# Kernel tuning notes

Measured on AMD Instinct MI355X. Metric: run time of the kernel, lower is better.

The kernel has to match this reference:

```python
import jax, jax.numpy as jnp
import numpy as np
from jax import lax


def _conv(x, w, b, pad, dil):
    # standard dense conv, NCHW / OIHW
    out = lax.conv_general_dilated(
        x, w, window_strides=(1, 1), padding=[(pad, pad), (pad, pad)],
        rhs_dilation=(dil, dil), dimension_numbers=('NCHW', 'OIHW', 'NCHW'))
    return out + b[None, :, None, None]


def _bilinear_sample(x, py, px):
    # x: [B,C,H,W]; py,px: [B,H,W] float coords. Zero padding outside bounds
    # (matches torchvision deform_conv2d bilinear sampling).
    B, C, H, W = x.shape
    y0 = jnp.floor(py)
    x0 = jnp.floor(px)
    wy = (py - y0)[:, None]  # [B,1,H,W]
    wx = (px - x0)[:, None]
    y0i = y0.astype(jnp.int32)
    x0i = x0.astype(jnp.int32)
    xf = x.reshape(B, C, H * W)

    def gather(yi, xi):
        valid = ((yi >= 0) & (yi < H) & (xi >= 0) & (xi < W))[:, None]
        yc = jnp.clip(yi, 0, H - 1)
        xc = jnp.clip(xi, 0, W - 1)
        idx = jnp.broadcast_to((yc * W + xc).reshape(B, 1, H * W), (B, C, H * W))
        v = jnp.take_along_axis(xf, idx, axis=2).reshape(B, C, H, W)
        return v * valid.astype(x.dtype)

    v00 = gather(y0i, x0i)
    v01 = gather(y0i, x0i + 1)
    v10 = gather(y0i + 1, x0i)
    v11 = gather(y0i + 1, x0i + 1)
    return (v00 * (1 - wy) * (1 - wx) + v01 * (1 - wy) * wx
            + v10 * wy * (1 - wx) + v11 * wy * wx)


def _deform_dw_conv(x, off_w, off_b, dw_w, k, pad, dil):
    # offset net: regular conv -> [B, 2*k*k, H, W] (dy,dx per kernel tap)
    # then depthwise deformable conv with weight dw_w: [C,1,k,k], no bias.
    B, C, H, W = x.shape
    off = _conv(x, off_w, off_b, pad, dil).reshape(B, k * k, 2, H, W)
    ys = jnp.arange(H, dtype=x.dtype)[None, :, None]  # [1,H,1]
    xs = jnp.arange(W, dtype=x.dtype)[None, None, :]  # [1,1,W]
    out = jnp.zeros_like(x)
    for t in range(k * k):  # small fixed tap count (25 or 49)
        ki, kj = t // k, t % k
        py = ys - pad + ki * dil + off[:, t, 0]  # [B,H,W]
        px = xs - pad + kj * dil + off[:, t, 1]
        samp = _bilinear_sample(x, py, px)       # [B,C,H,W]
        out = out + samp * dw_w[:, 0, ki, kj][None, :, None, None]
    return out


def setup_inputs() -> dict:
    key = jax.random.key(0)
    ks = jax.random.split(key, 10)
    B, C, H, W = 8, 64, 128, 128
    x = jax.random.normal(ks[0], (B, C, H, W), dtype=jnp.float32)
    # conv0: DeformConv 5x5, pad=2, dil=1, depthwise
    off0_w = jax.random.normal(ks[1], (2 * 25, C, 5, 5), dtype=jnp.float32) * 0.01
    off0_b = jnp.zeros((2 * 25,), dtype=jnp.float32)
    dw0_w = jax.random.normal(ks[2], (C, 1, 5, 5), dtype=jnp.float32) * (1.0 / 5.0)
    # conv_spatial: DeformConv 7x7, pad=9, dil=3, depthwise
    off1_w = jax.random.normal(ks[3], (2 * 49, C, 7, 7), dtype=jnp.float32) * 0.01
    off1_b = jnp.zeros((2 * 49,), dtype=jnp.float32)
    dw1_w = jax.random.normal(ks[4], (C, 1, 7, 7), dtype=jnp.float32) * (1.0 / 7.0)
    # conv1: 1x1 dense conv with bias
    conv1_w = jax.random.normal(ks[5], (C, C, 1, 1), dtype=jnp.float32) * (1.0 / np.sqrt(C))
    conv1_b = jnp.zeros((C,), dtype=jnp.float32)
    return {"x": x, "off0_w": off0_w, "off0_b": off0_b, "dw0_w": dw0_w,
            "off1_w": off1_w, "off1_b": off1_b, "dw1_w": dw1_w,
            "conv1_w": conv1_w, "conv1_b": conv1_b}


def reference(x, off0_w, off0_b, dw0_w, off1_w, off1_b, dw1_w, conv1_w, conv1_b):
    u = x
    attn = _deform_dw_conv(x, off0_w, off0_b, dw0_w, k=5, pad=2, dil=1)
    attn = _deform_dw_conv(attn, off1_w, off1_b, dw1_w, k=7, pad=9, dil=3)
    attn = jnp.einsum('bchw,oc->bohw', attn, conv1_w[:, :, 0, 0]) + conv1_b[None, :, None, None]
    return u * attn
```

## Files before the change

### kernel.cpp

```cpp
#include <hip/hip_runtime.h>
#include <hip/hip_fp16.h>

#define Bb 8
#define C  64
#define Hh 128
#define Ww 128
#define HW (Hh * Ww)

typedef __attribute__((ext_vector_type(8))) short b16x8;
typedef __attribute__((ext_vector_type(4))) float f32x4;
typedef _Float16 f16x8 __attribute__((ext_vector_type(8)));
typedef __fp16 fp16x2cv __attribute__((ext_vector_type(2)));

__device__ __forceinline__ ushort f2h(float f) {
    union { _Float16 h; ushort u; } z; z.h = (_Float16)f; return z.u;
}
__device__ __forceinline__ uint pkrtz_u(float a, float b) {
    union { fp16x2cv h; uint u; } z;
    z.h = __builtin_amdgcn_cvt_pkrtz(a, b); return z.u;
}
__device__ __forceinline__ f16x8 s2h8(b16x8 s) {
    union { b16x8 s; f16x8 h; } x; x.s = s; return x.h;
}
__device__ __forceinline__ __half2 u2hh(uint u) {
    union { uint u; __half2 h; } x; x.u = u; return x.h;
}
__device__ __forceinline__ uint hh2u(__half2 h) {
    union { uint u; __half2 h; } x; x.h = h; return x.u;
}
__device__ __forceinline__ float h2f_lo(uint u) {
    union { uint u; __half2 h; } x; x.u = u; return __low2float(x.h);
}
__device__ __forceinline__ float h2f_hi(uint u) {
    union { uint u; __half2 h; } x; x.u = u; return __high2float(x.h);
}

__global__ void pack_nhwc(const float* __restrict__ in, ushort* __restrict__ out) {
    __shared__ ushort t[64][65];
    const int bx = blockIdx.x;
    const int b = bx >> 8, rem = bx & 255, h = rem >> 1, w0 = (rem & 1) << 6;
    const int x = threadIdx.x, wl = x & 63, cs = x >> 6;
    const float* ip = in + (((size_t)b * 64) << 14) + (h << 7) + w0 + wl;
    #pragma unroll
    for (int i = 0; i < 16; ++i) {
        const int c = i * 4 + cs;
        t[wl][c] = f2h(ip[(size_t)c << 14]);
    }
    __syncthreads();
    ushort* op = out + ((size_t)((b * Hh + h) * Ww + w0)) * 64 + wl;
    #pragma unroll
    for (int i = 0; i < 16; ++i) {
        const int w = i * 4 + cs;
        op[(size_t)w * 64] = t[w][wl];
    }
}

__global__ void pack_w(const float* __restrict__ src, ushort* __restrict__ dst,
                       int OC, int OCP, int KK, int n) {
    const int idx = blockIdx.x * 256 + threadIdx.x;
    if (idx >= n) return;
    const int kk = idx & 31;
    const int oc = (idx >> 5) % OCP;
    const int s = idx / (32 * OCP);
    const int c = (s & 1) * 32 + kk;
    const int t = s >> 1;
    const float v = (oc < OC) ? src[((size_t)oc * 64 + c) * KK + t] : 0.f;
    dst[idx] = f2h(v);
}

__global__ void pack_dwt(const float* __restrict__ src, ushort* __restrict__ dst, int KK) {
    const int i = blockIdx.x * 256 + threadIdx.x;
    if (i < KK * 64) {
        const int t = i >> 6, ch = i & 63;
        dst[i] = f2h(src[ch * KK + t]);
    }
}

template<int K, int PAD, int DIL, int OCP, int KR>
__global__ __launch_bounds__(256, 4) void conv_mfma(
    const ushort* __restrict__ xp,
    const ushort* __restrict__ wp,
    const float* __restrict__ bias,
    ushort* __restrict__ outp) {
    constexpr int WIDTH = 128 + (K - 1) * DIL;
    constexpr int S = 2 * K * K;
    constexpr int SP = S + 2;
    constexpr int NT = OCP / 16;
    constexpr int TPW = (NT + 3) / 4;
    constexpr int STG = KR * WIDTH * 64;
    constexpr int EPI = 128 * SP;
    constexpr int LN = STG > EPI ? STG : EPI;
    __shared__ __align__(16) ushort lds[LN];

    const int bx = blockIdx.x;
    const int b = bx >> 7, h = bx & 127;
    const int tid = threadIdx.x, lane = tid & 63, wid = tid >> 6;
    const int l15 = lane & 15, lg = lane >> 4;

    f32x4 acc[TPW][8] = {};

    const int nph = (K + KR - 1) / KR;
    for (int ph = 0; ph < nph; ++ph) {
        const int kr0 = ph * KR;
        const int krn = (K - kr0 < KR) ? (K - kr0) : KR;
        __syncthreads();
        const int chunks = krn * WIDTH * 8;
        for (int q = tid; q < chunks; q += 256) {
            const int ki = q / (WIDTH * 8);
            const int r2 = q - ki * (WIDTH * 8);
            const int widx = r2 >> 3, csl = r2 & 7;
            const int y = h - PAD + (kr0 + ki) * DIL;
            const int w = -PAD + widx;
            uint4 v = make_uint4(0, 0, 0, 0);
            if ((unsigned)y < 128u && (unsigned)w < 128u)
                v = *(const uint4*)(xp + (((size_t)(b * 128 + y) * 128 + w) << 6) + (csl << 3));
            ((uint4*)lds)[(ki * WIDTH + widx) * 8 + (csl ^ (widx & 7))] = v;
        }
        __syncthreads();

        const int t1 = (kr0 + krn) * K;
        for (int t = kr0 * K; t < t1; ++t) {
            const int ki = t / K - kr0;
            const int kj = t - (t / K) * K;
            const int s0 = 2 * t;
            b16x8 a[2][TPW];
            #pragma unroll
            for (int i = 0; i < TPW; ++i) {
                if (wid + 4 * i < NT) {
                    const int ot = wid + 4 * i;
                    const size_t ab = ((size_t)(ot * 16 + l15)) * 32 + lg * 8;
                    a[0][i] = *(const b16x8*)(wp + (size_t)s0 * (OCP * 32) + ab);
                    a[1][i] = *(const b16x8*)(wp + (size_t)(s0 + 1) * (OCP * 32) + ab);
                }
            }
            const int wb0 = l15 + kj * DIL;
            int idx = (ki * WIDTH + wb0) * 8 + (lg ^ (wb0 & 7));
            #pragma unroll
            for (int pt = 0; pt < 8; ++pt) {
                const b16x8 b0 = ((const b16x8*)lds)[idx];
                const b16x8 b1 = ((const b16x8*)lds)[idx ^ 4];
                #pragma unroll
                for (int i = 0; i < TPW; ++i) {
                    if (wid + 4 * i < NT) {
                        acc[i][pt] = __builtin_amdgcn_mfma_f32_16x16x32_f16(s2h8(a[0][i]), s2h8(b0), acc[i][pt], 0, 0, 0);
                        acc[i][pt] = __builtin_amdgcn_mfma_f32_16x16x32_f16(s2h8(a[1][i]), s2h8(b1), acc[i][pt], 0, 0, 0);
                    }
                }
                idx += 128;
            }
        }
    }

    __syncthreads();
    #pragma unroll
    for (int i = 0; i < TPW; ++i) {
        const int ot = wid + 4 * i;
        if (ot >= NT) continue;
        #pragma unroll
        for (int r = 0; r < 4; ++r) {
            const int oc = ot * 16 + lg * 4 + r;
            if (oc < S) {
                const float bv = bias[oc];
                #pragma unroll
                for (int pt = 0; pt < 8; ++pt)
                    lds[(pt * 16 + l15) * SP + oc] = f2h(acc[i][pt][r] + bv);
            }
        }
    }
    __syncthreads();
    constexpr int SH = S / 2, SPH = SP / 2;
    const uint* lu = (const uint*)lds;
    uint* og = (uint*)outp + ((size_t)bx << 7) * SH;
    for (int q = tid; q < 128 * SH; q += 256) {
        const int pix = q / SH, s = q - pix * SH;
        og[q] = lu[pix * SPH + s];
    }
}

template <int K, int PAD, int DIL>
__global__ __launch_bounds__(512) void deform6(
    const ushort* __restrict__ xp,
    const ushort* __restrict__ off,
    const ushort* __restrict__ dwt,
    ushort* __restrict__ outb) {
    constexpr int KK = K * K;
    constexpr int H0 = (KK + 1) / 2;
    constexpr int SSTB = 32 * KK * 16;
    __shared__ __align__(16) char smem[SSTB + KK * 128];
    uint4* sST = (uint4*)smem;
    ushort* dwl = (ushort*)(smem + SSTB);

    const int tid = threadIdx.x;
    const int pix0 = blockIdx.x * 32;

    for (int i = tid; i < KK * 32; i += 512)
        ((uint*)dwl)[i] = ((const uint*)dwt)[i];

    const uint* og = (const uint*)off + (size_t)pix0 * KK;
    for (int q = tid; q < 32 * KK; q += 512) {
        const int pl2 = q / KK, t2 = q - pl2 * KK;
        const int pix = pix0 + pl2;
        const int h = (pix >> 7) & 127, w = pix & 127;
        const uint od = og[q];
        const int ki = t2 / K, kj = t2 - ki * K;
        const float py = (float)(h - PAD + ki * DIL) + h2f_lo(od);
        const float px = (float)(w - PAD + kj * DIL) + h2f_hi(od);
        const float y0f = floorf(py), x0f = floorf(px);
        const float wy = py - y0f, wx = px - x0f;
        const int y0 = (int)y0f, x0 = (int)x0f;
        const int y1 = y0 + 1, x1 = x0 + 1;
        const float m00 = ((unsigned)y0 < 128u && (unsigned)x0 < 128u) ? 1.f : 0.f;
        const float m01 = ((unsigned)y0 < 128u && (unsigned)x1 < 128u) ? 1.f : 0.f;
        const float m10 = ((unsigned)y1 < 128u && (unsigned)x0 < 128u) ? 1.f : 0.f;
        const float m11 = ((unsigned)y1 < 128u && (unsigned)x1 < 128u) ? 1.f : 0.f;
        const int y0c = min(max(y0, 0), 127), y1c = min(max(y1, 0), 127);
        const int x0c = min(max(x0, 0), 127), x1c = min(max(x1, 0), 127);
        const float w00 = (1.f - wy) * (1.f - wx) * m00;
        const float w01 = (1.f - wy) * wx * m01;
        const float w10 = wy * (1.f - wx) * m10;
        const float w11 = wy * wx * m11;
        const uint o00b = (uint)(((y0c << 7) | x0c) << 7);
        const uint o11b = (uint)(((y1c << 7) | x1c) << 7);
        const uint dxf = (uint)(x1c - x0c) << 24;
        sST[q] = make_uint4(o00b | dxf, o11b,
                            pkrtz_u(w00, w01), pkrtz_u(w10, w11));
    }
    __syncthreads();

    const int g = tid & 7, pl = (tid >> 3) & 31, half = tid >> 8;
    const int pix = pix0 + pl;
    const int bimg = pix0 >> 14;
    const int gb2 = g << 4;
    const char* xb8 = (const char*)xp + ((size_t)bimg << 21);
    const int base = pl * KK;
    const int t0 = half ? H0 : 0, t1 = half ? KK : H0;

    __half2 acc_h[4] = {};

    for (int tt = t0; tt < t1; ++tt) {
        const uint4 st = sST[base + tt];
        const uint a = st.x;
        const uint o00 = (a & 0x00FFFFFFu) + gb2;
        const uint dxb = (a >> 17) & 128u;
        const uint o11 = st.y + gb2;
        const __half2 wv0 = u2hh(st.z), wv1 = u2hh(st.w);
        const __half2 w00b = __low2half2(wv0), w01b = __high2half2(wv0);
        const __half2 w10b = __low2half2(wv1), w11b = __high2half2(wv1);
        const uint4 qa = *(const uint4*)(xb8 + o00);
        const uint4 qb = *(const uint4*)(xb8 + (o00 + dxb));
        const uint4 qc = *(const uint4*)(xb8 + (o11 - dxb));
        const uint4 qd = *(const uint4*)(xb8 + o11);
        const uint4 dwv = *(const uint4*)(dwl + (tt << 6) + (g << 3));
        const uint* Ap = (const uint*)&qa;
        const uint* Bp = (const uint*)&qb;
        const uint* Cp = (const uint*)&qc;
        const uint* Dp = (const uint*)&qd;
        const uint* Wp = (const uint*)&dwv;
        #pragma unroll
        for (int j = 0; j < 4; ++j) {
            __half2 v = __hmul2(u2hh(Ap[j]), w00b);
            v = __hfma2(u2hh(Bp[j]), w01b, v);
            v = __hfma2(u2hh(Cp[j]), w10b, v);
            v = __hfma2(u2hh(Dp[j]), w11b, v);
            acc_h[j] = __hfma2(v, u2hh(Wp[j]), acc_h[j]);
        }
    }

    __syncthreads();
    uint4* red = (uint4*)smem;
    if (half) {
        red[tid & 255] = make_uint4(hh2u(acc_h[0]), hh2u(acc_h[1]),
                                    hh2u(acc_h[2]), hh2u(acc_h[3]));
    }
    __syncthreads();
    if (!half) {
        const uint4 o = red[tid];
        acc_h[0] = __hadd2(acc_h[0], u2hh(o.x));
        acc_h[1] = __hadd2(acc_h[1], u2hh(o.y));
        acc_h[2] = __hadd2(acc_h[2], u2hh(o.z));
        acc_h[3] = __hadd2(acc_h[3], u2hh(o.w));
        uint o4[4];
        #pragma unroll
        for (int j = 0; j < 4; ++j) o4[j] = hh2u(acc_h[j]);
        *(uint4*)(outb + ((size_t)pix << 6) + (g << 3)) = *(uint4*)o4;
    }
}

__global__ __launch_bounds__(256) void pw_mfma(
    const ushort* __restrict__ attn, const ushort* __restrict__ wp2,
    const float* __restrict__ b1, const float* __restrict__ x,
    float* __restrict__ out) {
    __shared__ __align__(16) ushort lds[64 * 64];
    const int tid = threadIdx.x, lane = tid & 63, wid = tid >> 6;
    const int l15 = lane & 15, lg = lane >> 4;
    const int pix0 = blockIdx.x << 6;

    const uint4* src = (const uint4*)(attn + ((size_t)pix0 << 6));
    for (int q = tid; q < 512; q += 256) {
        const int widx = q >> 3, csl = q & 7;
        ((uint4*)lds)[widx * 8 + (csl ^ (widx & 7))] = src[q];
    }
    __syncthreads();

    const b16x8 a0 = *(const b16x8*)(wp2 + ((size_t)(wid * 16 + l15)) * 32 + lg * 8);
    const b16x8 a1 = *(const b16x8*)(wp2 + ((size_t)(64 + wid * 16 + l15)) * 32 + lg * 8);
    f32x4 acc[4] = {};
    #pragma unroll
    for (int pt = 0; pt < 4; ++pt) {
        const int wb = pt * 16 + l15;
        const int idx = wb * 8 + (lg ^ (wb & 7));
        const b16x8 b0 = ((const b16x8*)lds)[idx];
        const b16x8 b1v = ((const b16x8*)lds)[idx ^ 4];
        acc[pt] = __builtin_amdgcn_mfma_f32_16x16x32_f16(s2h8(a0), s2h8(b0), acc[pt], 0, 0, 0);
        acc[pt] = __builtin_amdgcn_mfma_f32_16x16x32_f16(s2h8(a1), s2h8(b1v), acc[pt], 0, 0, 0);
    }

    const int b = pix0 >> 14, hw0 = pix0 & 16383;
    #pragma unroll
    for (int r = 0; r < 4; ++r) {
        const int oc = wid * 16 + lg * 4 + r;
        const float bv = b1[oc];
        const size_t base = (((size_t)b * 64 + oc) << 14) + hw0;
        #pragma unroll
        for (int pt = 0; pt < 4; ++pt) {
            const size_t oi = base + pt * 16 + l15;
            out[oi] = x[oi] * (acc[pt][r] + bv);
        }
    }
}

extern "C" void kernel_launch(void* const* d_in, const int* in_sizes, int n_in,
                              void* d_out, int out_size, void* d_ws, size_t ws_size,
                              hipStream_t stream) {
    const float* x       = (const float*)d_in[0];
    const float* off0_w  = (const float*)d_in[1];
    const float* off0_b  = (const float*)d_in[2];
    const float* dw0_w   = (const float*)d_in[3];
    const float* off1_w  = (const float*)d_in[4];
    const float* off1_b  = (const float*)d_in[5];
    const float* dw1_w   = (const float*)d_in[6];
    const float* conv1_w = (const float*)d_in[7];
    const float* conv1_b = (const float*)d_in[8];
    float* out = (float*)d_out;

    const size_t NPX = (size_t)Bb * HW;
    ushort* xp     = (ushort*)d_ws;
    ushort* attn0b = xp + NPX * 64;
    ushort* attn1b = attn0b + NPX * 64;
    ushort* offb   = attn1b + NPX * 64;
    ushort* wp0    = offb + NPX * 98;
    ushort* wp1    = wp0 + 50 * 64 * 32;
    ushort* wpP    = wp1 + 98 * 112 * 32;
    ushort* dwt0   = wpP + 2 * 64 * 32;
    ushort* dwt1   = dwt0 + 25 * 64;

    const dim3 blk(256);

    pack_nhwc<<<2048, blk, 0, stream>>>(x, xp);
    pack_w<<<(50 * 64 * 32 + 255) / 256, blk, 0, stream>>>(off0_w, wp0, 50, 64, 25, 50 * 64 * 32);
    pack_w<<<(98 * 112 * 32 + 255) / 256, blk, 0, stream>>>(off1_w, wp1, 98, 112, 49, 98 * 112 * 32);
    pack_w<<<16, blk, 0, stream>>>(conv1_w, wpP, 64, 64, 1, 2 * 64 * 32);
    pack_dwt<<<(25 * 64 + 255) / 256, blk, 0, stream>>>(dw0_w, dwt0, 25);
    pack_dwt<<<(49 * 64 + 255) / 256, blk, 0, stream>>>(dw1_w, dwt1, 49);

    conv_mfma<5, 2, 1, 64, 2><<<1024, blk, 0, stream>>>(xp, wp0, off0_b, offb);
    deform6<5, 2, 1><<<4096, 512, 0, stream>>>(xp, offb, dwt0, attn0b);

    conv_mfma<7, 9, 3, 112, 2><<<1024, blk, 0, stream>>>(attn0b, wp1, off1_b, offb);
    deform6<7, 9, 3><<<4096, 512, 0, stream>>>(attn0b, offb, dwt1, attn1b);

    pw_mfma<<<2048, blk, 0, stream>>>(attn1b, wpP, conv1_b, x, out);
}
```

Baseline: 311.6 us.

## Restructure deformable sampling to 64 pixels per block without tap split; merge pack kernels

Measured after the change: 302.2 us. -3.0%, faster.

```diff
diff --git a/kernel.cpp b/kernel.cpp
--- a/kernel.cpp
+++ b/kernel.cpp
@@ -55,10 +55,8 @@
     }
 }
 
-__global__ void pack_w(const float* __restrict__ src, ushort* __restrict__ dst,
-                       int OC, int OCP, int KK, int n) {
-    const int idx = blockIdx.x * 256 + threadIdx.x;
-    if (idx >= n) return;
+__device__ __forceinline__ void do_pack_w(const float* src, ushort* dst,
+                                          int OC, int OCP, int KK, int idx) {
     const int kk = idx & 31;
     const int oc = (idx >> 5) % OCP;
     const int s = idx / (32 * OCP);
@@ -67,13 +65,30 @@
     const float v = (oc < OC) ? src[((size_t)oc * 64 + c) * KK + t] : 0.f;
     dst[idx] = f2h(v);
 }
-
-__global__ void pack_dwt(const float* __restrict__ src, ushort* __restrict__ dst, int KK) {
-    const int i = blockIdx.x * 256 + threadIdx.x;
-    if (i < KK * 64) {
-        const int t = i >> 6, ch = i & 63;
-        dst[i] = f2h(src[ch * KK + t]);
-    }
+__global__ void pack_all(const float* __restrict__ off0_w, ushort* __restrict__ wp0,
+                         const float* __restrict__ off1_w, ushort* __restrict__ wp1,
+                         const float* __restrict__ conv1_w, ushort* __restrict__ wpP,
+                         const float* __restrict__ dw0_w, ushort* __restrict__ dwt0,
+                         const float* __restrict__ dw1_w, ushort* __restrict__ dwt1) {
+    const int N0 = 50 * 2 * 64 * 32;
+    const int n0 = 2 * 25 * 64 * 32;
+    const int n1 = 2 * 49 * 112 * 32;
+    const int n2 = 2 * 64 * 32;
+    const int n3 = 25 * 64;
+    const int n4 = 49 * 64;
+    (void)N0;
+    int idx = blockIdx.x * 256 + threadIdx.x;
+    if (idx < n0) { do_pack_w(off0_w, wp0, 50, 64, 25, idx); return; }
+    idx -= n0;
+    if (idx < n1) { do_pack_w(off1_w, wp1, 98, 112, 49, idx); return; }
+    idx -= n1;
+    if (idx < n2) { do_pack_w(conv1_w, wpP, 64, 64, 1, idx); return; }
+    idx -= n2;
+    if (idx < n3) { const int t = idx >> 6, ch = idx & 63;
+                    dwt0[idx] = f2h(dw0_w[ch * 25 + t]); return; }
+    idx -= n3;
+    if (idx < n4) { const int t = idx >> 6, ch = idx & 63;
+                    dwt1[idx] = f2h(dw1_w[ch * 49 + t]); }
 }
 
 template<int K, int PAD, int DIL, int OCP, int KR>
@@ -178,26 +193,24 @@
 }
 
 template <int K, int PAD, int DIL>
-__global__ __launch_bounds__(512) void deform6(
+__global__ __launch_bounds__(512) void deform7k(
     const ushort* __restrict__ xp,
     const ushort* __restrict__ off,
     const ushort* __restrict__ dwt,
     ushort* __restrict__ outb) {
     constexpr int KK = K * K;
-    constexpr int H0 = (KK + 1) / 2;
-    constexpr int SSTB = 32 * KK * 16;
-    __shared__ __align__(16) char smem[SSTB + KK * 128];
-    uint4* sST = (uint4*)smem;
-    ushort* dwl = (ushort*)(smem + SSTB);
-
+    __shared__ uint sIdx[64 * KK];
+    __shared__ __align__(8) uint2 sW[64 * KK];
+    __shared__ ushort dwl[KK * 64];
     const int tid = threadIdx.x;
-    const int pix0 = blockIdx.x * 32;
+    const int img = blockIdx.x & 7;
+    const int pix0 = img * HW + (blockIdx.x >> 3) * 64;
 
     for (int i = tid; i < KK * 32; i += 512)
         ((uint*)dwl)[i] = ((const uint*)dwt)[i];
 
     const uint* og = (const uint*)off + (size_t)pix0 * KK;
-    for (int q = tid; q < 32 * KK; q += 512) {
+    for (int q = tid; q < 64 * KK; q += 512) {
         const int pl2 = q / KK, t2 = q - pl2 * KK;
         const int pix = pix0 + pl2;
         const int h = (pix >> 7) & 127, w = pix & 127;
@@ -219,31 +232,30 @@
         const float w01 = (1.f - wy) * wx * m01;
         const float w10 = wy * (1.f - wx) * m10;
         const float w11 = wy * wx * m11;
-        const uint o00b = (uint)(((y0c << 7) | x0c) << 7);
-        const uint o11b = (uint)(((y1c << 7) | x1c) << 7);
-        const uint dxf = (uint)(x1c - x0c) << 24;
-        sST[q] = make_uint4(o00b | dxf, o11b,
-                            pkrtz_u(w00, w01), pkrtz_u(w10, w11));
-    }
-    __syncthreads();
-
-    const int g = tid & 7, pl = (tid >> 3) & 31, half = tid >> 8;
+        const int i00 = (y0c << 7) | x0c;
+        const int i11 = (y1c << 7) | x1c;
+        const int dx = x1c - x0c;
+        sIdx[q] = (uint)i00 | ((uint)i11 << 14) | ((uint)dx << 28);
+        sW[q] = make_uint2(pkrtz_u(w00, w01), pkrtz_u(w10, w11));
+    }
+    __syncthreads();
+
+    const int g = tid & 7, pl = tid >> 3;
     const int pix = pix0 + pl;
-    const int bimg = pix0 >> 14;
     const int gb2 = g << 4;
-    const char* xb8 = (const char*)xp + ((size_t)bimg << 21);
+    const char* xb8 = (const char*)xp + ((size_t)img << 21);
     const int base = pl * KK;
-    const int t0 = half ? H0 : 0, t1 = half ? KK : H0;
 
     __half2 acc_h[4] = {};
 
-    for (int tt = t0; tt < t1; ++tt) {
-        const uint4 st = sST[base + tt];
-        const uint a = st.x;
-        const uint o00 = (a & 0x00FFFFFFu) + gb2;
-        const uint dxb = (a >> 17) & 128u;
-        const uint o11 = st.y + gb2;
-        const __half2 wv0 = u2hh(st.z), wv1 = u2hh(st.w);
+    #pragma unroll 2
+    for (int tt = 0; tt < KK; ++tt) {
+        const uint id = sIdx[base + tt];
+        const uint2 w4 = sW[base + tt];
+        const uint o00 = ((id & 16383u) << 7) + gb2;
+        const uint o11 = (((id >> 14) & 16383u) << 7) + gb2;
+        const uint dxb = (id >> 21) & 128u;
+        const __half2 wv0 = u2hh(w4.x), wv1 = u2hh(w4.y);
         const __half2 w00b = __low2half2(wv0), w01b = __high2half2(wv0);
         const __half2 w10b = __low2half2(wv1), w11b = __high2half2(wv1);
         const uint4 qa = *(const uint4*)(xb8 + o00);
@@ -266,24 +278,10 @@
         }
     }
 
-    __syncthreads();
-    uint4* red = (uint4*)smem;
-    if (half) {
-        red[tid & 255] = make_uint4(hh2u(acc_h[0]), hh2u(acc_h[1]),
-                                    hh2u(acc_h[2]), hh2u(acc_h[3]));
-    }
-    __syncthreads();
-    if (!half) {
-        const uint4 o = red[tid];
-        acc_h[0] = __hadd2(acc_h[0], u2hh(o.x));
-        acc_h[1] = __hadd2(acc_h[1], u2hh(o.y));
-        acc_h[2] = __hadd2(acc_h[2], u2hh(o.z));
-        acc_h[3] = __hadd2(acc_h[3], u2hh(o.w));
-        uint o4[4];
-        #pragma unroll
-        for (int j = 0; j < 4; ++j) o4[j] = hh2u(acc_h[j]);
-        *(uint4*)(outb + ((size_t)pix << 6) + (g << 3)) = *(uint4*)o4;
-    }
+    uint o4[4];
+    #pragma unroll
+    for (int j = 0; j < 4; ++j) o4[j] = hh2u(acc_h[j]);
+    *(uint4*)(outb + ((size_t)pix << 6) + (g << 3)) = *(uint4*)o4;
 }
 
 __global__ __launch_bounds__(256) void pw_mfma(
@@ -357,17 +355,14 @@
     const dim3 blk(256);
 
     pack_nhwc<<<2048, blk, 0, stream>>>(x, xp);
-    pack_w<<<(50 * 64 * 32 + 255) / 256, blk, 0, stream>>>(off0_w, wp0, 50, 64, 25, 50 * 64 * 32);
-    pack_w<<<(98 * 112 * 32 + 255) / 256, blk, 0, stream>>>(off1_w, wp1, 98, 112, 49, 98 * 112 * 32);
-    pack_w<<<16, blk, 0, stream>>>(conv1_w, wpP, 64, 64, 1, 2 * 64 * 32);
-    pack_dwt<<<(25 * 64 + 255) / 256, blk, 0, stream>>>(dw0_w, dwt0, 25);
-    pack_dwt<<<(49 * 64 + 255) / 256, blk, 0, stream>>>(dw1_w, dwt1, 49);
+    pack_all<<<(462464 + 255) / 256, blk, 0, stream>>>(
+        off0_w, wp0, off1_w, wp1, conv1_w, wpP, dw0_w, dwt0, dw1_w, dwt1);
 
     conv_mfma<5, 2, 1, 64, 2><<<1024, blk, 0, stream>>>(xp, wp0, off0_b, offb);
-    deform6<5, 2, 1><<<4096, 512, 0, stream>>>(xp, offb, dwt0, attn0b);
+    deform7k<5, 2, 1><<<2048, 512, 0, stream>>>(xp, offb, dwt0, attn0b);
 
     conv_mfma<7, 9, 3, 112, 2><<<1024, blk, 0, stream>>>(attn0b, wp1, off1_b, offb);
-    deform6<7, 9, 3><<<4096, 512, 0, stream>>>(attn0b, offb, dwt1, attn1b);
+    deform7k<7, 9, 3><<<2048, 512, 0, stream>>>(attn0b, offb, dwt1, attn1b);
 
     pw_mfma<<<2048, blk, 0, stream>>>(attn1b, wpP, conv1_b, x, out);
 }
```
